# Performance work log

Measured on AMD Instinct MI355X. Metric: run time of the kernel, lower is better.

Reference implementation:

```python
import jax, jax.numpy as jnp
import numpy as np

S = 8192      # total packed tokens
H = 1152      # hidden size
NH = 16       # heads
HD = 72       # head dim
NSEG = 8      # number of packed (equal-length) sequences
L = S // NSEG # tokens per sequence
SCALE = HD ** -0.5


def setup_inputs() -> dict:
    key = jax.random.key(0)
    ks = jax.random.split(key, 4)
    hidden_states = jax.random.normal(ks[0], (1, S, H), jnp.float32)
    # Real rotary cos/sin per token position within each sequence.
    inv_freq = 1.0 / (10000.0 ** (np.arange(0, HD, 2, dtype=np.float64) / HD))
    freqs = np.outer(np.arange(L, dtype=np.float64), inv_freq)  # [L, HD/2]
    emb = np.concatenate([freqs, freqs], axis=-1)               # [L, HD]
    cos = jnp.asarray(np.tile(np.cos(emb), (NSEG, 1)), jnp.float32)  # [S, HD]
    sin = jnp.asarray(np.tile(np.sin(emb), (NSEG, 1)), jnp.float32)
    Wqkv = jax.random.normal(ks[1], (H, 3 * H), jnp.float32) * (H ** -0.5)
    bqkv = jnp.zeros((3 * H,), jnp.float32)
    Wout = jax.random.normal(ks[2], (H, H), jnp.float32) * (H ** -0.5)
    bout = jnp.zeros((H,), jnp.float32)
    cu_seqlens = jnp.arange(NSEG + 1, dtype=jnp.int32) * L
    return dict(hidden_states=hidden_states, cos=cos, sin=sin,
                Wqkv=Wqkv, bqkv=bqkv, Wout=Wout, bout=bout,
                cu_seqlens=cu_seqlens)


def _rotate_half(x):
    return jnp.concatenate([-x[..., HD // 2:], x[..., :HD // 2]], axis=-1)


def reference(hidden_states, cos, sin, Wqkv, bqkv, Wout, bout, cu_seqlens):
    # QKV projection (fused)
    qkv = hidden_states @ Wqkv + bqkv                 # [1, S, 3H]
    q, k, v = jnp.split(qkv, [H, 2 * H], axis=-1)
    q = q.reshape(1, S, NH, HD)
    k = k.reshape(1, S, NH, HD)
    v = v.reshape(1, S, NH, HD)
    # Inline RoPE on q/k (cos/sin broadcast over heads)
    c = cos[None, :, None, :]
    s = sin[None, :, None, :]
    q = q * c + _rotate_half(q) * s
    k = k * c + _rotate_half(k) * s
    # Varlen (block-diagonal) non-causal attention: equal-length segments
    q = q.reshape(NSEG, L, NH, HD)
    k = k.reshape(NSEG, L, NH, HD)
    v = v.reshape(NSEG, L, NH, HD)
    scores = jnp.einsum('nqhd,nkhd->nhqk', q, k) * SCALE  # [NSEG, NH, L, L]
    probs = jax.nn.softmax(scores, axis=-1)
    ctx = jnp.einsum('nhqk,nkhd->nqhd', probs, v)         # [NSEG, L, NH, HD]
    ctx = ctx.reshape(1, S, H)
    # Output projection
    return ctx @ Wout + bout
```

## Files before the change

### kernel.cpp

```cpp
#include <hip/hip_runtime.h>
#include <hip/hip_fp16.h>
#include <cstdint>

typedef _Float16 half8 __attribute__((ext_vector_type(8)));
typedef _Float16 half4 __attribute__((ext_vector_type(4)));
typedef float floatx4 __attribute__((ext_vector_type(4)));

#define S_TOT 8192
#define H_DIM 1152
#define NHEAD 16
#define HD 72
#define QSTR 96
#define KSTR 104
#define PSTR 76
#define VSTR 76
#define VT_TILE 6080
#define NSEG 8
#define SEGL 1024
#define QSCALE 0.17002324631230988f

__device__ __forceinline__ void gld_lds16(const void* g, void* l) {
  __builtin_amdgcn_global_load_lds((const __attribute__((address_space(1))) void*)g,
                                   (__attribute__((address_space(3))) void*)l, 16, 0, 0);
}

__global__ void cast_f32_f16(const float* __restrict__ in, _Float16* __restrict__ out, int n) {
  int i = (blockIdx.x * 256 + threadIdx.x) * 4;
  if (i < n) {
    float4 v = *(const float4*)(in + i);
    half4 o = { (_Float16)v.x, (_Float16)v.y, (_Float16)v.z, (_Float16)v.w };
    *(half4*)(out + i) = o;
  }
}

__global__ void transpose_cast(const float* __restrict__ W, _Float16* __restrict__ Wt,
                               int R, int C) {
  __shared__ float tile[32][33];
  int tx = threadIdx.x, ty = threadIdx.y;
  int bx = blockIdx.x, by = blockIdx.y;
#pragma unroll
  for (int i = 0; i < 4; ++i)
    tile[ty + i * 8][tx] = W[(size_t)(by * 32 + ty + i * 8) * C + bx * 32 + tx];
  __syncthreads();
#pragma unroll
  for (int i = 0; i < 4; ++i)
    Wt[(size_t)(bx * 32 + ty + i * 8) * R + by * 32 + tx] = (_Float16)tile[tx][ty + i * 8];
}

template <bool OUT_HALF>
__global__ __launch_bounds__(512, 2) void gemm256(
    const _Float16* __restrict__ A, const _Float16* __restrict__ Bt,
    const float* __restrict__ bias, float* __restrict__ Cf, _Float16* __restrict__ Ch,
    int M, int N, int K, int NT) {
  extern __shared__ half8 smem8[];
  char* smem = (char*)smem8;
  const int tid = threadIdx.x;
  const int lane = tid & 63;
  const int w = tid >> 6;
  const int quad = lane >> 4, l16 = lane & 15;
  const int wm = w >> 2, wn = w & 3;

  const int orig = blockIdx.x;
  const int xcd = orig & 7, widx = orig >> 3;
  const int mt = xcd * 4 + (widx & 3), nt = widx >> 2;
  const int m0 = mt * 256, n0 = nt * 256;

  const _Float16* pA[2];
  const _Float16* pB[2];
#pragma unroll
  for (int i = 0; i < 2; ++i) {
    int c = i * 512 + tid;
    int r = c >> 2, cs = c & 3;
    int col = ((cs ^ ((r >> 1) & 3)) << 3);
    pA[i] = A + (size_t)(m0 + r) * K + col;
    int br = n0 + r; if (br >= N) br = N - 1;
    pB[i] = Bt + (size_t)br * K + col;
  }
  const int st0 = tid * 16, st1 = tid * 16 + 8192;
  const int rsl = ((quad ^ ((l16 >> 1) & 3)) << 4);
  const int aoff = (wm * 128 + l16) * 64 + rsl;
  const int boff = 16384 + (wn * 64 + l16) * 64 + rsl;

  half8 afA[8], bfA[4], afB[8], bfB[4];
  floatx4 acc[8][4] = {};

#define STG_A(ds, kcol) { \
  gld_lds16(pA[0] + (kcol), smem + (ds) * 32768 + st0); \
  gld_lds16(pA[1] + (kcol), smem + (ds) * 32768 + st1); }
#define STG_B(ds, kcol) { \
  gld_lds16(pB[0] + (kcol), smem + (ds) * 32768 + 16384 + st0); \
  gld_lds16(pB[1] + (kcol), smem + (ds) * 32768 + 16384 + st1); }
#define LDB4(s, bfx) { \
  _Pragma("unroll") for (int in = 0; in < 4; ++in) \
    bfx[in] = *(const half8*)(smem + (s) * 32768 + boff + in * 1024); }
#define LDA8(s, afx) { \
  _Pragma("unroll") for (int j = 0; j < 8; ++j) \
    afx[j] = *(const half8*)(smem + (s) * 32768 + aoff + j * 1024); }
#define MFMA32(afx, bfx) { \
  __builtin_amdgcn_s_setprio(1); \
  _Pragma("unroll") for (int j = 0; j < 8; ++j) \
  _Pragma("unroll") for (int in = 0; in < 4; ++in) \
    acc[j][in] = \
      __builtin_amdgcn_mfma_f32_16x16x32_f16(afx[j], bfx[in], acc[j][in], 0, 0, 0); \
  __builtin_amdgcn_s_setprio(0); }
#define BAR() __builtin_amdgcn_s_barrier()
#define SBAR() __builtin_amdgcn_sched_barrier(0)
#define LGKM0() { asm volatile("s_waitcnt lgkmcnt(0)" ::: "memory"); SBAR(); }
#define VMWAIT(t) { \
  if ((t) + 3 < KT)        { asm volatile("s_waitcnt vmcnt(4)" ::: "memory"); } \
  else if ((t) + 3 == KT)  { asm volatile("s_waitcnt vmcnt(0)" ::: "memory"); } }

  STG_A(0, 0);  STG_B(0, 0);
  STG_A(1, 32); STG_B(1, 32);
  STG_A(2, 64); STG_B(2, 64);
  asm volatile("s_waitcnt vmcnt(4)" ::: "memory");
  BAR();
  LDB4(0, bfA); LDA8(0, afA);
  LGKM0();

  const int KT = K >> 5;
#pragma unroll 1
  for (int u = 0; u < KT; u += 2) {
    {
      const int rs = (u + 1) & 3, ws = (u + 3) & 3;
      LDB4(rs, bfB); LDA8(rs, afB);
      if (u + 3 < KT) { STG_A(ws, (u + 3) * 32); STG_B(ws, (u + 3) * 32); }
      SBAR();
      MFMA32(afA, bfA);
      SBAR();
      LGKM0();
      VMWAIT(u);
      BAR();
    }
    {
      const int rs = (u + 2) & 3, ws = (u + 4) & 3;
      if (u + 2 < KT) { LDB4(rs, bfA); LDA8(rs, afA); }
      if (u + 4 < KT) { STG_A(ws, (u + 4) * 32); STG_B(ws, (u + 4) * 32); }
      SBAR();
      MFMA32(afB, bfB);
      SBAR();
      LGKM0();
      VMWAIT(u + 1);
      if (u + 2 < KT) BAR();
    }
  }
#undef STG_A
#undef STG_B
#undef LDB4
#undef LDA8
#undef MFMA32
#undef BAR
#undef SBAR
#undef LGKM0
#undef VMWAIT

#pragma unroll
  for (int im = 0; im < 8; ++im) {
    int m = m0 + wm * 128 + im * 16 + quad * 4;
#pragma unroll
    for (int in = 0; in < 4; ++in) {
      int n = n0 + wn * 64 + in * 16 + l16;
      if (n < N) {
        float b = bias[n];
#pragma unroll
        for (int r = 0; r < 4; ++r) {
          float v = acc[im][in][r] + b;
          if (OUT_HALF) Ch[(size_t)(m + r) * N + n] = (_Float16)v;
          else          Cf[(size_t)(m + r) * N + n] = v;
        }
      }
    }
  }
}

__global__ __launch_bounds__(256) void rope_scatter(
    const _Float16* __restrict__ QKV,
    const float* __restrict__ cosb,
    const float* __restrict__ sinb,
    _Float16* __restrict__ Qo, _Float16* __restrict__ Ko) {
  __shared__ __align__(16) _Float16 Ls[256 * 120];
  const int tid = threadIdx.x;
  const int t0 = blockIdx.x * 256;
  const int t = t0 + tid;
  const int l = t & 1023, h = (t >> 10) & 15, n = t >> 14;
  const int s = n * SEGL + l;
  const _Float16* q = QKV + (size_t)s * 3456 + h * HD;
  const _Float16* k = q + H_DIM;
  const float* cs = cosb + (size_t)s * HD;
  const float* sn = sinb + (size_t)s * HD;
  half8 z = {};
  {
    _Float16 qr[72], qv[72];
#pragma unroll
    for (int i = 0; i < 9; ++i) *(half8*)&qr[8 * i] = *(const half8*)(q + 8 * i);
#pragma unroll
    for (int d = 0; d < 36; ++d) {
      float c0 = cs[d], s0 = sn[d], c1 = cs[d + 36], s1 = sn[d + 36];
      float a = (float)qr[d], b = (float)qr[d + 36];
      qv[d]      = (_Float16)((a * c0 - b * s0) * QSCALE);
      qv[d + 36] = (_Float16)((b * c1 + a * s1) * QSCALE);
    }
#pragma unroll
    for (int i = 0; i < 9; ++i) *(half8*)&Ls[tid * 104 + 8 * i] = *(half8*)&qv[8 * i];
#pragma unroll
    for (int i = 9; i < 12; ++i) *(half8*)&Ls[tid * 104 + 8 * i] = z;
  }
  __syncthreads();
  {
    _Float16* dst = Qo + (size_t)t0 * QSTR;
#pragma unroll
    for (int it = 0; it < 12; ++it) {
      int j = tid + it * 256;
      int row = j / 12, c = j - row * 12;
      *(half8*)(dst + (size_t)j * 8) = *(const half8*)&Ls[row * 104 + c * 8];
    }
  }
  __syncthreads();
  {
    _Float16 kr[72], kv[72];
#pragma unroll
    for (int i = 0; i < 9; ++i) *(half8*)&kr[8 * i] = *(const half8*)(k + 8 * i);
#pragma unroll
    for (int d = 0; d < 36; ++d) {
      float c0 = cs[d], s0 = sn[d], c1 = cs[d + 36], s1 = sn[d + 36];
      float a = (float)kr[d], b = (float)kr[d + 36];
      kv[d]      = (_Float16)(a * c0 - b * s0);
      kv[d + 36] = (_Float16)(b * c1 + a * s1);
    }
#pragma unroll
    for (int i = 0; i < 9; ++i) *(half8*)&Ls[tid * 120 + 8 * i] = *(half8*)&kv[8 * i];
#pragma unroll
    for (int i = 9; i < 13; ++i) *(half8*)&Ls[tid * 120 + 8 * i] = z;
  }
  __syncthreads();
  {
    _Float16* dst = Ko + (size_t)t0 * KSTR;
#pragma unroll
    for (int it = 0; it < 13; ++it) {
      int j = tid + it * 256;
      int row = j / 13, c = j - row * 13;
      *(half8*)(dst + (size_t)j * 8) = *(const half8*)&Ls[row * 120 + c * 8];
    }
  }
}

__global__ __launch_bounds__(256) void transpose_v(const _Float16* __restrict__ QKV,
                                                   _Float16* __restrict__ Vt) {
  __shared__ __align__(16) _Float16 Vs[64 * 88];
  const int tid = threadIdx.x;
  const int kb = blockIdx.x, h = blockIdx.y, n = blockIdx.z;
  const int s0 = n * SEGL + kb * 64;
  const _Float16* src = QKV + (size_t)s0 * 3456 + 2 * H_DIM + h * HD;
  for (int idx = tid; idx < 576; idx += 256) {
    int key = idx / 9, c = idx - key * 9;
    *(half8*)&Vs[key * 88 + c * 8] = *(const half8*)(src + (size_t)key * 3456 + c * 8);
  }
  __syncthreads();
  _Float16* dst = Vt + (((size_t)(n * NHEAD + h)) * 16 + kb) * VT_TILE;
  for (int idx = tid; idx < 800; idx += 256) {
    int d = idx / 10, c = idx - d * 10;
    if (c < 8) {
      half8 v = {};
      if (d < HD) {
#pragma unroll
        for (int j = 0; j < 8; ++j) v[j] = Vs[(c * 8 + j) * 88 + d];
      } else if (d == HD) {
#pragma unroll
        for (int j = 0; j < 8; ++j) v[j] = (_Float16)1.0f;
      }
      *(half8*)(dst + d * VSTR + c * 8) = v;
    } else if (c == 8) {
      *(half8*)(dst + d * VSTR + 64) = half8{};
    } else {
      *(half4*)(dst + d * VSTR + 72) = half4{};
    }
  }
}

__global__ __launch_bounds__(256, 3) void attn_kernel(
    const _Float16* __restrict__ Qb, const _Float16* __restrict__ Kb,
    const _Float16* __restrict__ Vtb, _Float16* __restrict__ Ctx) {
  __shared__ __align__(16) _Float16 Kt[64 * KSTR];
  __shared__ __align__(16) _Float16 Vt[80 * VSTR];
  __shared__ __align__(16) _Float16 Ps[4 * 16 * PSTR];
  const int tid = threadIdx.x;
  const int lane = tid & 63, w = tid >> 6;
  const int quad = lane >> 4, l16 = lane & 15;
  const int id = blockIdx.x;
  const int hn = id & 127, qb = id >> 7;
  const int h = hn >> 3, n = hn & 7;
  const size_t hseg = (size_t)(n * NHEAD + h);
  const _Float16* Qg = Qb + hseg * SEGL * QSTR;
  const _Float16* Kg = Kb + hseg * SEGL * KSTR;
  const _Float16* Vg = Vtb + hseg * 16 * VT_TILE;

  half8 qf[2][3];
#pragma unroll
  for (int qg = 0; qg < 2; ++qg) {
    int row = qb * 128 + w * 32 + qg * 16 + l16;
#pragma unroll
    for (int kc = 0; kc < 3; ++kc)
      qf[qg][kc] = *(const half8*)(Qg + (size_t)row * QSTR + kc * 32 + quad * 8);
  }
  floatx4 o_acc[2][5] = {};

  for (int kb = 0; kb < SEGL / 64; ++kb) {
    __syncthreads();
    {
      const char* base = (const char*)(Kg + (size_t)kb * 64 * KSTR);
#pragma unroll
      for (int i = 0; i < 3; ++i)
        gld_lds16(base + tid * 16 + i * 4096, (char*)Kt + tid * 16 + i * 4096);
      if (tid < 64)
        gld_lds16(base + 12288 + tid * 16, (char*)Kt + 12288 + tid * 16);
    }
    {
      const char* base = (const char*)(Vg + (size_t)kb * VT_TILE);
#pragma unroll
      for (int i = 0; i < 2; ++i)
        gld_lds16(base + tid * 16 + i * 4096, (char*)Vt + tid * 16 + i * 4096);
      if (tid < 248)
        gld_lds16(base + 8192 + tid * 16, (char*)Vt + 8192 + tid * 16);
    }
    __syncthreads();
    floatx4 sa[2][4] = {};
    __builtin_amdgcn_s_setprio(1);
#pragma unroll
    for (int nt = 0; nt < 4; ++nt) {
      half8 kf[3];
#pragma unroll
      for (int kc = 0; kc < 3; ++kc)
        kf[kc] = *(const half8*)&Kt[(nt * 16 + l16) * KSTR + kc * 32 + quad * 8];
#pragma unroll
      for (int qg = 0; qg < 2; ++qg)
#pragma unroll
        for (int kc = 0; kc < 3; ++kc)
          sa[qg][nt] = __builtin_amdgcn_mfma_f32_16x16x32_f16(kf[kc], qf[qg][kc], sa[qg][nt], 0, 0, 0);
    }
    __builtin_amdgcn_s_setprio(0);
#pragma unroll
    for (int qg = 0; qg < 2; ++qg)
#pragma unroll
      for (int nt = 0; nt < 4; ++nt)
#pragma unroll
        for (int r = 0; r < 4; ++r)
          sa[qg][nt][r] = exp2f(sa[qg][nt][r]);
    half8 vf[2][5];
#pragma unroll
    for (int kc2 = 0; kc2 < 2; ++kc2)
#pragma unroll
      for (int t = 0; t < 5; ++t)
        vf[kc2][t] = *(const half8*)&Vt[(t * 16 + l16) * VSTR + kc2 * 32 + quad * 8];
#pragma unroll
    for (int qg = 0; qg < 2; ++qg) {
      int prow = (w * 16 + l16) * PSTR;
#pragma unroll
      for (int nt = 0; nt < 4; ++nt) {
        half4 ph = { (_Float16)sa[qg][nt][0], (_Float16)sa[qg][nt][1],
                     (_Float16)sa[qg][nt][2], (_Float16)sa[qg][nt][3] };
        *(half4*)&Ps[prow + nt * 16 + quad * 4] = ph;
      }
      __builtin_amdgcn_s_setprio(1);
#pragma unroll
      for (int kc2 = 0; kc2 < 2; ++kc2) {
        half8 pb = *(const half8*)&Ps[(w * 16 + l16) * PSTR + kc2 * 32 + quad * 8];
#pragma unroll
        for (int t = 0; t < 5; ++t)
          o_acc[qg][t] = __builtin_amdgcn_mfma_f32_16x16x32_f16(vf[kc2][t], pb, o_acc[qg][t], 0, 0, 0);
      }
      __builtin_amdgcn_s_setprio(0);
    }
  }
#pragma unroll
  for (int qg = 0; qg < 2; ++qg) {
    float lsum = __shfl(o_acc[qg][4][0], 32 + l16, 64);
    float rl = 1.0f / lsum;
    size_t s2 = (size_t)n * SEGL + qb * 128 + w * 32 + qg * 16 + l16;
#pragma unroll
    for (int t = 0; t < 5; ++t) {
      int d0 = t * 16 + quad * 4;
      if (d0 < HD) {
        half4 hv = { (_Float16)(o_acc[qg][t][0] * rl), (_Float16)(o_acc[qg][t][1] * rl),
                     (_Float16)(o_acc[qg][t][2] * rl), (_Float16)(o_acc[qg][t][3] * rl) };
        *(half4*)&Ctx[s2 * H_DIM + h * HD + d0] = hv;
      }
    }
  }
}

extern "C" void kernel_launch(void* const* d_in, const int* in_sizes, int n_in,
                              void* d_out, int out_size, void* d_ws, size_t ws_size,
                              hipStream_t stream) {
  const float* X    = (const float*)d_in[0];
  const float* cosb = (const float*)d_in[1];
  const float* sinb = (const float*)d_in[2];
  const float* Wqkv = (const float*)d_in[3];
  const float* bqkv = (const float*)d_in[4];
  const float* Wout = (const float*)d_in[5];
  const float* bout = (const float*)d_in[6];
  float* out = (float*)d_out;
  char* ws = (char*)d_ws;

  _Float16* Xb   = (_Float16*)(ws);
  _Float16* Wqt  = (_Float16*)(ws + 18874368);
  _Float16* Wot  = (_Float16*)(ws + 26836992);
  _Float16* QKVb = (_Float16*)(ws + 29491200);
  _Float16* Qb   = (_Float16*)(ws + 86114304);
  _Float16* Kb   = (_Float16*)(ws + 111280128);
  _Float16* Vtb  = (_Float16*)(ws + 138543104);
  _Float16* Ctx  = Xb;

  static bool attr_done = false;
  if (!attr_done) {
    hipFuncSetAttribute(reinterpret_cast<const void*>(gemm256<true>),
                        hipFuncAttributeMaxDynamicSharedMemorySize, 131072);
    hipFuncSetAttribute(reinterpret_cast<const void*>(gemm256<false>),
                        hipFuncAttributeMaxDynamicSharedMemorySize, 131072);
    attr_done = true;
  }

  cast_f32_f16<<<9216, 256, 0, stream>>>(X, Xb, S_TOT * H_DIM);
  transpose_cast<<<dim3(108, 36), dim3(32, 8), 0, stream>>>(Wqkv, Wqt, H_DIM, 3 * H_DIM);
  transpose_cast<<<dim3(36, 36), dim3(32, 8), 0, stream>>>(Wout, Wot, H_DIM, H_DIM);
  gemm256<true><<<448, 512, 131072, stream>>>(Xb, Wqt, bqkv, nullptr, QKVb,
                                              S_TOT, 3 * H_DIM, H_DIM, 14);
  rope_scatter<<<512, 256, 0, stream>>>(QKVb, cosb, sinb, Qb, Kb);
  transpose_v<<<dim3(16, 16, 8), 256, 0, stream>>>(QKVb, Vtb);
  attn_kernel<<<1024, 256, 0, stream>>>(Qb, Kb, Vtb, Ctx);
  gemm256<false><<<160, 512, 131072, stream>>>(Ctx, Wot, bout, out, nullptr,
                                               S_TOT, H_DIM, H_DIM, 5);
}
```

Measured before the change: 359.6 us.

## Double-buffer K/V tiles in attention and use smaller-tile GEMM for output projection

The attention kernel now keeps two K/V staging slots in dynamic shared memory and issues the async load for the next key block before computing on the current one. This overlaps global-to-LDS transfer with MFMA work and drops one barrier per iteration. In exchange, LDS use rises and occupancy falls from 3 to 2 blocks per CU. The output projection moves from the 256-tile GEMM (160 blocks) to a new 128x128-tile GEMM with 576 blocks, to fill more CUs on the narrow N=1152 matrix.

```diff
diff --git a/kernel.cpp b/kernel.cpp
--- a/kernel.cpp
+++ b/kernel.cpp
@@ -173,6 +173,78 @@
   }
 }
 
+template <bool OUT_HALF>
+__global__ __launch_bounds__(256) void gemm_bt(
+    const _Float16* __restrict__ A, const _Float16* __restrict__ Bt,
+    const float* __restrict__ bias, float* __restrict__ Cf, _Float16* __restrict__ Ch,
+    int M, int N, int K, int NT) {
+  __shared__ __align__(16) _Float16 As[128 * 72];
+  __shared__ __align__(16) _Float16 Bs[128 * 72];
+  const int tid = threadIdx.x;
+  const int lane = tid & 63, w = tid >> 6;
+  const int quad = lane >> 4, l16 = lane & 15;
+  const int wm = w >> 1, wn = w & 1;
+  const int id = blockIdx.x;
+  const int j = id & 7, k = id >> 3;
+  const int nt_ = k % NT, mt_ = (k / NT) * 8 + j;
+  const int m0 = mt_ * 128, n0 = nt_ * 128;
+
+  int rowi[5], cci[5];
+#pragma unroll
+  for (int i = 0; i < 5; ++i) {
+    int c = tid + i * 256;
+    int r = c / 9, cc = c - r * 9;
+    rowi[i] = r;
+    cci[i] = (cc == 8) ? 0 : cc;
+  }
+
+  floatx4 acc[4][4] = {};
+
+  for (int kt = 0; kt < K; kt += 64) {
+    __syncthreads();
+#pragma unroll
+    for (int i = 0; i < 4; ++i) {
+      gld_lds16(A + (size_t)(m0 + rowi[i]) * K + kt + cci[i] * 8, (char*)As + (tid + i * 256) * 16);
+      gld_lds16(Bt + (size_t)(n0 + rowi[i]) * K + kt + cci[i] * 8, (char*)Bs + (tid + i * 256) * 16);
+    }
+    if (tid < 128) {
+      gld_lds16(A + (size_t)(m0 + rowi[4]) * K + kt + cci[4] * 8, (char*)As + (tid + 1024) * 16);
+      gld_lds16(Bt + (size_t)(n0 + rowi[4]) * K + kt + cci[4] * 8, (char*)Bs + (tid + 1024) * 16);
+    }
+    __syncthreads();
+#pragma unroll
+    for (int kk = 0; kk < 2; ++kk) {
+      half8 af[4], bf[4];
+#pragma unroll
+      for (int im = 0; im < 4; ++im)
+        af[im] = *(const half8*)&As[(wm * 64 + im * 16 + l16) * 72 + kk * 32 + quad * 8];
+#pragma unroll
+      for (int in = 0; in < 4; ++in)
+        bf[in] = *(const half8*)&Bs[(wn * 64 + in * 16 + l16) * 72 + kk * 32 + quad * 8];
+#pragma unroll
+      for (int im = 0; im < 4; ++im)
+#pragma unroll
+        for (int in = 0; in < 4; ++in)
+          acc[im][in] = __builtin_amdgcn_mfma_f32_16x16x32_f16(af[im], bf[in], acc[im][in], 0, 0, 0);
+    }
+  }
+#pragma unroll
+  for (int im = 0; im < 4; ++im) {
+    int m = m0 + wm * 64 + im * 16 + quad * 4;
+#pragma unroll
+    for (int in = 0; in < 4; ++in) {
+      int n = n0 + wn * 64 + in * 16 + l16;
+      float b = bias[n];
+#pragma unroll
+      for (int r = 0; r < 4; ++r) {
+        float v = acc[im][in][r] + b;
+        if (OUT_HALF) Ch[(size_t)(m + r) * N + n] = (_Float16)v;
+        else          Cf[(size_t)(m + r) * N + n] = v;
+      }
+    }
+  }
+}
+
 __global__ __launch_bounds__(256) void rope_scatter(
     const _Float16* __restrict__ QKV,
     const float* __restrict__ cosb,
@@ -277,12 +349,10 @@
   }
 }
 
-__global__ __launch_bounds__(256, 3) void attn_kernel(
+__global__ __launch_bounds__(256, 2) void attn_kernel(
     const _Float16* __restrict__ Qb, const _Float16* __restrict__ Kb,
     const _Float16* __restrict__ Vtb, _Float16* __restrict__ Ctx) {
-  __shared__ __align__(16) _Float16 Kt[64 * KSTR];
-  __shared__ __align__(16) _Float16 Vt[80 * VSTR];
-  __shared__ __align__(16) _Float16 Ps[4 * 16 * PSTR];
+  extern __shared__ __align__(16) char asmem[];
   const int tid = threadIdx.x;
   const int lane = tid & 63, w = tid >> 6;
   const int quad = lane >> 4, l16 = lane & 15;
@@ -293,6 +363,23 @@
   const _Float16* Qg = Qb + hseg * SEGL * QSTR;
   const _Float16* Kg = Kb + hseg * SEGL * KSTR;
   const _Float16* Vg = Vtb + hseg * 16 * VT_TILE;
+  _Float16* Ps = (_Float16*)(asmem + 57344);
+
+  auto STAGE = [&](int kb2, int slot) {
+    const char* kbase = (const char*)(Kg + (size_t)kb2 * 64 * KSTR);
+    char* kdst = asmem + slot * 28672;
+    gld_lds16(kbase + tid * 16,         kdst + tid * 16);
+    gld_lds16(kbase + tid * 16 + 4096,  kdst + tid * 16 + 4096);
+    gld_lds16(kbase + tid * 16 + 8192,  kdst + tid * 16 + 8192);
+    int ko = tid * 16 + 12288; if (ko > 13296) ko = 13296;
+    gld_lds16(kbase + ko,               kdst + tid * 16 + 12288);
+    const char* vbase = (const char*)(Vg + (size_t)kb2 * VT_TILE);
+    char* vdst = kdst + 16384;
+    gld_lds16(vbase + tid * 16,         vdst + tid * 16);
+    gld_lds16(vbase + tid * 16 + 4096,  vdst + tid * 16 + 4096);
+    int vo = tid * 16 + 8192; if (vo > 12144) vo = 12144;
+    gld_lds16(vbase + vo,               vdst + tid * 16 + 8192);
+  };
 
   half8 qf[2][3];
 #pragma unroll
@@ -304,25 +391,12 @@
   }
   floatx4 o_acc[2][5] = {};
 
+  STAGE(0, 0);
   for (int kb = 0; kb < SEGL / 64; ++kb) {
     __syncthreads();
-    {
-      const char* base = (const char*)(Kg + (size_t)kb * 64 * KSTR);
-#pragma unroll
-      for (int i = 0; i < 3; ++i)
-        gld_lds16(base + tid * 16 + i * 4096, (char*)Kt + tid * 16 + i * 4096);
-      if (tid < 64)
-        gld_lds16(base + 12288 + tid * 16, (char*)Kt + 12288 + tid * 16);
-    }
-    {
-      const char* base = (const char*)(Vg + (size_t)kb * VT_TILE);
-#pragma unroll
-      for (int i = 0; i < 2; ++i)
-        gld_lds16(base + tid * 16 + i * 4096, (char*)Vt + tid * 16 + i * 4096);
-      if (tid < 248)
-        gld_lds16(base + 8192 + tid * 16, (char*)Vt + 8192 + tid * 16);
-    }
-    __syncthreads();
+    if (kb < SEGL / 64 - 1) STAGE(kb + 1, (kb + 1) & 1);
+    const _Float16* Kt = (const _Float16*)(asmem + (kb & 1) * 28672);
+    const _Float16* Vt = (const _Float16*)(asmem + (kb & 1) * 28672 + 16384);
     floatx4 sa[2][4] = {};
     __builtin_amdgcn_s_setprio(1);
 #pragma unroll
@@ -414,8 +488,8 @@
   if (!attr_done) {
     hipFuncSetAttribute(reinterpret_cast<const void*>(gemm256<true>),
                         hipFuncAttributeMaxDynamicSharedMemorySize, 131072);
-    hipFuncSetAttribute(reinterpret_cast<const void*>(gemm256<false>),
-                        hipFuncAttributeMaxDynamicSharedMemorySize, 131072);
+    hipFuncSetAttribute(reinterpret_cast<const void*>(attn_kernel),
+                        hipFuncAttributeMaxDynamicSharedMemorySize, 67072);
     attr_done = true;
   }
 
@@ -426,7 +500,7 @@
                                               S_TOT, 3 * H_DIM, H_DIM, 14);
   rope_scatter<<<512, 256, 0, stream>>>(QKVb, cosb, sinb, Qb, Kb);
   transpose_v<<<dim3(16, 16, 8), 256, 0, stream>>>(QKVb, Vtb);
-  attn_kernel<<<1024, 256, 0, stream>>>(Qb, Kb, Vtb, Ctx);
-  gemm256<false><<<160, 512, 131072, stream>>>(Ctx, Wot, bout, out, nullptr,
-                                               S_TOT, H_DIM, H_DIM, 5);
-}
+  attn_kernel<<<1024, 256, 67072, stream>>>(Qb, Kb, Vtb, Ctx);
+  gemm_bt<false><<<576, 256, 0, stream>>>(Ctx, Wot, bout, out, nullptr,
+                                          S_TOT, H_DIM, H_DIM, 9);
+}
```

Result: slower. 419.0 us (+16.5%).
